# Kernel optimization log

Hardware: AMD Instinct MI355X
Metric: run time of the kernel (lower is better)

Reference implementation:

```python
import jax, jax.numpy as jnp
import numpy as np

ATOMS_PER_RES = 24  # hard-coded in .view(B, N_l, -1, 24)
NEG_SLOPE = 0.01    # nn.LeakyReLU default


def setup_inputs() -> dict:
    key = jax.random.key(0)
    ks = jax.random.split(key, 10)
    B, N_l, N_p, H, G = 16, 64, 512, 128, 10
    pos_l = jax.random.normal(ks[0], (B, N_l, 3), jnp.float32) * 5.0
    pos_p = jax.random.normal(ks[1], (B, N_p, ATOMS_PER_RES, 3), jnp.float32) * 5.0
    Interact = jax.random.normal(ks[2], (B, N_l, N_p, H), jnp.float32)
    Interact_mask = jax.random.randint(ks[3], (B, N_l, N_p), 0, 2) > 0
    W_pi = jax.random.normal(ks[4], (H, G), jnp.float32) * 0.05
    b_pi = jnp.zeros((G,), jnp.float32)
    W_sigma = jax.random.normal(ks[5], (H, G), jnp.float32) * 0.05
    b_sigma = jnp.zeros((G,), jnp.float32)
    W_mu = jax.random.normal(ks[6], (H, G), jnp.float32) * 0.05
    b_mu = jnp.zeros((G,), jnp.float32)
    return {
        "pos_l": pos_l, "pos_p": pos_p, "Interact": Interact,
        "Interact_mask": Interact_mask,
        "W_pi": W_pi, "b_pi": b_pi,
        "W_sigma": W_sigma, "b_sigma": b_sigma,
        "W_mu": W_mu, "b_mu": b_mu,
    }


def _min_dist(pos_l, pos_p):
    # pos_l: [B, N_l, 3]; pos_p: [B, N_p, 24, 3]
    B, N_l, _ = pos_l.shape
    Y = pos_p.reshape(B, -1, 3)  # [B, N_p*24, 3]
    d2 = (jnp.sum(pos_l * pos_l, axis=-1)[..., None]
          + jnp.sum(Y * Y, axis=-1)[:, None, :]
          - 2.0 * jnp.einsum('bic,bjc->bij', pos_l, Y))  # [B, N_l, N_p*24]
    dist = jnp.nan_to_num(jnp.sqrt(d2), nan=10000.0)
    # min over the 24 atoms of each residue -> [B, N_l, N_p]
    return dist.reshape(B, N_l, -1, ATOMS_PER_RES).min(axis=-1)


def reference(pos_l, pos_p, Interact, Interact_mask,
              W_pi, b_pi, W_sigma, b_sigma, W_mu, b_mu):
    leaky = lambda x: jax.nn.leaky_relu(x, NEG_SLOPE)
    dist = _min_dist(pos_l, pos_p)                       # [B, N_l, N_p]
    # original gathers dist[Interact_mask]; keep static shape, zero-fill masked-out
    dist_masked = jnp.where(Interact_mask, dist, 0.0)
    pi = jax.nn.softmax(Interact @ W_pi + b_pi, axis=-1)          # [B,N_l,N_p,G]
    sigma = jnp.clip(leaky(Interact @ W_sigma + b_sigma) + 1.1, 1e-6, None)
    mu = leaky(Interact @ W_mu + b_mu) + 1.0
    return pi, sigma, mu, dist_masked, Interact_mask
```

## Files before the change

### kernel.cpp

```cpp
#include <hip/hip_runtime.h>
#include <cmath>

#define NB 16
#define NL 64
#define NP 512
#define NH 128
#define NG 10
#define ROWS (NB * NL * NP)

#define OFF_PI    ((size_t)0)
#define OFF_SIGMA ((size_t)5242880)
#define OFF_MU    ((size_t)10485760)
#define OFF_DIST  ((size_t)15728640)
#define OFF_MASK  ((size_t)16252928)

typedef __attribute__((ext_vector_type(8))) short short8;
typedef __attribute__((ext_vector_type(4))) float f32x4;

__device__ __forceinline__ unsigned pk2(float a, float b) {
    unsigned ua = __float_as_uint(a);
    unsigned ub = __float_as_uint(b);
    ua = (ua + 0x7fffu + ((ua >> 16) & 1u)) >> 16;
    ub = (ub + 0x7fffu + ((ub >> 16) & 1u)) & 0xffff0000u;
    return ua | ub;
}

__global__ __launch_bounds__(512) void k_pack(
    const float* __restrict__ Wpi, const float* __restrict__ Wsg,
    const float* __restrict__ Wmu, uint4* __restrict__ tbl)
{
    int e    = threadIdx.x;
    int lane = e & 63;
    int n    = (e >> 6) & 1;
    int ks   = e >> 7;
    int lrow = lane & 15, lkg = lane >> 4;
    int col  = n * 16 + lrow;
    float w[8];
    #pragma unroll
    for (int j = 0; j < 8; ++j) {
        int k = ks * 32 + lkg * 8 + j;
        float v = 0.0f;
        if      (col < 10) v = Wpi[k * NG + col];
        else if (col < 20) v = Wsg[k * NG + col - 10];
        else if (col < 30) v = Wmu[k * NG + col - 20];
        w[j] = v;
    }
    uint4 u = {pk2(w[0], w[1]), pk2(w[2], w[3]),
               pk2(w[4], w[5]), pk2(w[6], w[7])};
    tbl[e] = u;
}

__global__ __launch_bounds__(256, 4) void k_fused(
    const float* __restrict__ pos_l,
    const float* __restrict__ pos_p,
    const int*   __restrict__ mask,
    const float* __restrict__ X,
    const uint4* __restrict__ wtbl,
    const float* __restrict__ bpi,
    const float* __restrict__ bsg,
    const float* __restrict__ bmu,
    float* __restrict__ out_pi,
    float* __restrict__ out_sg,
    float* __restrict__ out_mu,
    float* __restrict__ dist_out,
    float* __restrict__ mask_out)
{
    __shared__ __align__(16) float xs[256 * 32];
    __shared__ __align__(16) uint4 bt[512];

    const int tid  = threadIdx.x;
    const int wv   = tid >> 6;
    const int lane = tid & 63;
    const int lrow = lane & 15;
    const int lkg  = lane >> 4;
    const int idx  = blockIdx.x * 256 + tid;
    const size_t row0 = (size_t)blockIdx.x * 256;

    const int a_ = lane >> 3;
    const int b_ = lane & 7;
    const int wchunk = b_ ^ a_;
    const int wro    = wv * 8 + a_;
    const float* gsb = X + (row0 + wro) * NH + b_ * 4;

    uint4 bt0 = wtbl[tid];
    uint4 bt1 = wtbl[tid + 256];
    float4 pf[8];
    #pragma unroll
    for (int j = 0; j < 8; ++j)
        pf[j] = *(const float4*)(gsb + (size_t)j * 32 * NH);

    const int c0 = lrow, c1 = lrow + 16;
    const float bv0 = (c0 < 10) ? bpi[c0] : bsg[c0 - 10];
    const float bv1 = (c1 < 20) ? bsg[c1 - 10] : (c1 < 30 ? bmu[c1 - 20] : 0.0f);

    {
        int p  = idx & (NP - 1);
        int bl = idx >> 9;
        int b  = bl >> 6;

        const float* xl = pos_l + bl * 3;
        float x0 = xl[0], x1 = xl[1], x2 = xl[2];
        float qs = x0 * x0 + x1 * x1 + x2 * x2;

        const float4* yp = (const float4*)(pos_p + ((size_t)(b * NP + p)) * 72);

        float m2 = 1e30f;
        #pragma unroll
        for (int q = 0; q < 6; ++q) {
            float4 v0 = yp[q * 3 + 0];
            float4 v1 = yp[q * 3 + 1];
            float4 v2 = yp[q * 3 + 2];
            float c[12] = {v0.x, v0.y, v0.z, v0.w,
                           v1.x, v1.y, v1.z, v1.w,
                           v2.x, v2.y, v2.z, v2.w};
            #pragma unroll
            for (int a = 0; a < 4; ++a) {
                float yx = c[a * 3 + 0], yy = c[a * 3 + 1], yz = c[a * 3 + 2];
                float d2 = qs + (yx * yx + yy * yy + yz * yz)
                              - 2.0f * (x0 * yx + x1 * yy + x2 * yz);
                d2 = (d2 >= 0.0f) ? d2 : 1e8f;
                m2 = fminf(m2, d2);
            }
        }
        float m = sqrtf(m2);
        int mk = mask[idx];
        dist_out[idx] = mk ? m : 0.0f;
        mask_out[idx] = mk ? 1.0f : 0.0f;
    }

    bt[tid]       = bt0;
    bt[tid + 256] = bt1;
    #pragma unroll
    for (int j = 0; j < 8; ++j)
        *(float4*)&xs[(wro + j * 32) * 32 + wchunk * 4] = pf[j];
    __syncthreads();

    f32x4 acc[4][2];
    #pragma unroll
    for (int m = 0; m < 4; ++m) {
        acc[m][0] = (f32x4){bv0, bv0, bv0, bv0};
        acc[m][1] = (f32x4){bv1, bv1, bv1, bv1};
    }

    const int s7 = lrow & 7;
    #pragma unroll
    for (int t = 0; t < 4; ++t) {
        if (t < 3) {
            #pragma unroll
            for (int j = 0; j < 8; ++j)
                pf[j] = *(const float4*)(gsb + (size_t)j * 32 * NH
                                             + (t + 1) * 32);
        }
        short8 bf0 = __builtin_bit_cast(short8, bt[(t * 2 + 0) * 64 + lane]);
        short8 bf1 = __builtin_bit_cast(short8, bt[(t * 2 + 1) * 64 + lane]);

        #pragma unroll
        for (int m = 0; m < 4; ++m) {
            const int R = wv * 64 + m * 16 + lrow;
            float4 lo = *(const float4*)&xs[R * 32 + ((2 * lkg)     ^ s7) * 4];
            float4 hi = *(const float4*)&xs[R * 32 + ((2 * lkg + 1) ^ s7) * 4];
            uint4 ua = {pk2(lo.x, lo.y), pk2(lo.z, lo.w),
                        pk2(hi.x, hi.y), pk2(hi.z, hi.w)};
            short8 af = __builtin_bit_cast(short8, ua);
            acc[m][0] = __builtin_amdgcn_mfma_f32_16x16x32_bf16(af, bf0, acc[m][0], 0, 0, 0);
            acc[m][1] = __builtin_amdgcn_mfma_f32_16x16x32_bf16(af, bf1, acc[m][1], 0, 0, 0);
        }

        if (t < 3) {
            __syncthreads();
            #pragma unroll
            for (int j = 0; j < 8; ++j)
                *(float4*)&xs[(wro + j * 32) * 32 + wchunk * 4] = pf[j];
            __syncthreads();
        }
    }

    #pragma unroll
    for (int m = 0; m < 4; ++m)
        #pragma unroll
        for (int n = 0; n < 2; ++n)
            #pragma unroll
            for (int r = 0; r < 4; ++r) {
                int Rabs = wv * 64 + m * 16 + lkg * 4 + r;
                int ch   = n * 4 + (lrow >> 2);
                xs[Rabs * 32 + ((ch ^ (Rabs & 7)) * 4) + (lrow & 3)]
                    = acc[m][n][r];
            }

    float a[32];
    #pragma unroll
    for (int j = 0; j < 8; ++j)
        *(float4*)&a[4 * j] = *(const float4*)&xs[tid * 32 + ((j ^ (tid & 7)) * 4)];

    const size_t ro = (size_t)idx * NG;

    float mx = a[0];
    #pragma unroll
    for (int g = 1; g < NG; ++g) mx = fmaxf(mx, a[g]);
    float e[NG], ssum = 0.0f;
    #pragma unroll
    for (int g = 0; g < NG; ++g) { e[g] = __expf(a[g] - mx); ssum += e[g]; }
    float inv = 1.0f / ssum;
    #pragma unroll
    for (int g = 0; g < 5; ++g)
        *(float2*)&out_pi[ro + 2 * g] = make_float2(e[2 * g] * inv,
                                                    e[2 * g + 1] * inv);

    #pragma unroll
    for (int g = 0; g < 5; ++g) {
        float xa = a[10 + 2 * g], xb = a[10 + 2 * g + 1];
        float va = fmaxf((xa >= 0.0f ? xa : 0.01f * xa) + 1.1f, 1e-6f);
        float vb = fmaxf((xb >= 0.0f ? xb : 0.01f * xb) + 1.1f, 1e-6f);
        *(float2*)&out_sg[ro + 2 * g] = make_float2(va, vb);
    }

    #pragma unroll
    for (int g = 0; g < 5; ++g) {
        float xa = a[20 + 2 * g], xb = a[20 + 2 * g + 1];
        float va = (xa >= 0.0f ? xa : 0.01f * xa) + 1.0f;
        float vb = (xb >= 0.0f ? xb : 0.01f * xb) + 1.0f;
        *(float2*)&out_mu[ro + 2 * g] = make_float2(va, vb);
    }
}

extern "C" void kernel_launch(void* const* d_in, const int* in_sizes, int n_in,
                              void* d_out, int out_size, void* d_ws, size_t ws_size,
                              hipStream_t stream) {
    const float* pos_l    = (const float*)d_in[0];
    const float* pos_p    = (const float*)d_in[1];
    const float* Interact = (const float*)d_in[2];
    const int*   mask     = (const int*)  d_in[3];
    const float* Wpi      = (const float*)d_in[4];
    const float* bpi      = (const float*)d_in[5];
    const float* Wsg      = (const float*)d_in[6];
    const float* bsg      = (const float*)d_in[7];
    const float* Wmu      = (const float*)d_in[8];
    const float* bmu      = (const float*)d_in[9];

    float* out      = (float*)d_out;
    float* out_pi   = out + OFF_PI;
    float* out_sg   = out + OFF_SIGMA;
    float* out_mu   = out + OFF_MU;
    float* out_dist = out + OFF_DIST;
    float* out_mask = out + OFF_MASK;

    uint4* wtbl = (uint4*)d_ws;

    hipLaunchKernelGGL(k_pack, dim3(1), dim3(512), 0, stream,
                       Wpi, Wsg, Wmu, wtbl);
    hipLaunchKernelGGL(k_fused, dim3(ROWS / 256), dim3(256), 0, stream,
                       pos_l, pos_p, mask, Interact, wtbl,
                       bpi, bsg, bmu,
                       out_pi, out_sg, out_mu, out_dist, out_mask);
}
```

Baseline: 458.0 us.

## Stage bf16-packed activations in LDS in two halves, read weights from global

After: 432.0 us. 5.7% less time.

```diff
diff --git a/kernel.cpp b/kernel.cpp
--- a/kernel.cpp
+++ b/kernel.cpp
@@ -65,8 +65,8 @@
     float* __restrict__ dist_out,
     float* __restrict__ mask_out)
 {
-    __shared__ __align__(16) float xs[256 * 32];
-    __shared__ __align__(16) uint4 bt[512];
+    __shared__ __align__(16) char smem[32768];
+    float* cs = (float*)smem;
 
     const int tid  = threadIdx.x;
     const int wv   = tid >> 6;
@@ -76,22 +76,18 @@
     const int idx  = blockIdx.x * 256 + tid;
     const size_t row0 = (size_t)blockIdx.x * 256;
 
-    const int a_ = lane >> 3;
-    const int b_ = lane & 7;
-    const int wchunk = b_ ^ a_;
-    const int wro    = wv * 8 + a_;
-    const float* gsb = X + (row0 + wro) * NH + b_ * 4;
-
-    uint4 bt0 = wtbl[tid];
-    uint4 bt1 = wtbl[tid + 256];
-    float4 pf[8];
-    #pragma unroll
-    for (int j = 0; j < 8; ++j)
-        pf[j] = *(const float4*)(gsb + (size_t)j * 32 * NH);
-
-    const int c0 = lrow, c1 = lrow + 16;
-    const float bv0 = (c0 < 10) ? bpi[c0] : bsg[c0 - 10];
-    const float bv1 = (c1 < 20) ? bsg[c1 - 10] : (c1 < 30 ? bmu[c1 - 20] : 0.0f);
+    const int r0 = tid >> 4, c0 = tid & 15;
+    const float* gs = X + (row0 + r0) * NH + c0 * 4;
+    const int wbyte0 = r0 * 128 + ((((c0 >> 1) ^ (r0 & 7)) * 16) | ((c0 & 1) * 8));
+
+    float4 pf[16];
+    #pragma unroll
+    for (int j = 0; j < 16; ++j)
+        pf[j] = *(const float4*)(gs + (size_t)j * 16 * NH);
+
+    const int cc0 = lrow, cc1 = lrow + 16;
+    const float bv0 = (cc0 < 10) ? bpi[cc0] : bsg[cc0 - 10];
+    const float bv1 = (cc1 < 20) ? bsg[cc1 - 10] : (cc1 < 30 ? bmu[cc1 - 20] : 0.0f);
 
     {
         int p  = idx & (NP - 1);
@@ -128,11 +124,15 @@
         mask_out[idx] = mk ? 1.0f : 0.0f;
     }
 
-    bt[tid]       = bt0;
-    bt[tid + 256] = bt1;
-    #pragma unroll
-    for (int j = 0; j < 8; ++j)
-        *(float4*)&xs[(wro + j * 32) * 32 + wchunk * 4] = pf[j];
+    {
+        uint2 pc[16];
+        #pragma unroll
+        for (int j = 0; j < 16; ++j)
+            pc[j] = make_uint2(pk2(pf[j].x, pf[j].y), pk2(pf[j].z, pf[j].w));
+        #pragma unroll
+        for (int j = 0; j < 16; ++j)
+            *(uint2*)(smem + wbyte0 + j * 2048) = pc[j];
+    }
     __syncthreads();
 
     f32x4 acc[4][2];
@@ -143,37 +143,43 @@
     }
 
     const int s7 = lrow & 7;
-    #pragma unroll
-    for (int t = 0; t < 4; ++t) {
-        if (t < 3) {
-            #pragma unroll
-            for (int j = 0; j < 8; ++j)
-                pf[j] = *(const float4*)(gsb + (size_t)j * 32 * NH
-                                             + (t + 1) * 32);
-        }
-        short8 bf0 = __builtin_bit_cast(short8, bt[(t * 2 + 0) * 64 + lane]);
-        short8 bf1 = __builtin_bit_cast(short8, bt[(t * 2 + 1) * 64 + lane]);
-
-        #pragma unroll
-        for (int m = 0; m < 4; ++m) {
-            const int R = wv * 64 + m * 16 + lrow;
-            float4 lo = *(const float4*)&xs[R * 32 + ((2 * lkg)     ^ s7) * 4];
-            float4 hi = *(const float4*)&xs[R * 32 + ((2 * lkg + 1) ^ s7) * 4];
-            uint4 ua = {pk2(lo.x, lo.y), pk2(lo.z, lo.w),
-                        pk2(hi.x, hi.y), pk2(hi.z, hi.w)};
-            short8 af = __builtin_bit_cast(short8, ua);
-            acc[m][0] = __builtin_amdgcn_mfma_f32_16x16x32_bf16(af, bf0, acc[m][0], 0, 0, 0);
-            acc[m][1] = __builtin_amdgcn_mfma_f32_16x16x32_bf16(af, bf1, acc[m][1], 0, 0, 0);
-        }
-
-        if (t < 3) {
-            __syncthreads();
-            #pragma unroll
-            for (int j = 0; j < 8; ++j)
-                *(float4*)&xs[(wro + j * 32) * 32 + wchunk * 4] = pf[j];
-            __syncthreads();
-        }
-    }
+    const char* abase = smem + wv * 8192 + lrow * 128;
+
+#define DO_KS(ksg, Cb)                                                        \
+    {                                                                         \
+        short8 bf0 = __builtin_bit_cast(short8, wtbl[((ksg) * 2 + 0) * 64 + lane]); \
+        short8 bf1 = __builtin_bit_cast(short8, wtbl[((ksg) * 2 + 1) * 64 + lane]); \
+        _Pragma("unroll")                                                     \
+        for (int m = 0; m < 4; ++m) {                                         \
+            short8 af = *(const short8*)(abase + m * 2048                     \
+                                         + ((((Cb)) ^ s7) * 16));             \
+            acc[m][0] = __builtin_amdgcn_mfma_f32_16x16x32_bf16(af, bf0, acc[m][0], 0, 0, 0); \
+            acc[m][1] = __builtin_amdgcn_mfma_f32_16x16x32_bf16(af, bf1, acc[m][1], 0, 0, 0); \
+        }                                                                     \
+    }
+
+    DO_KS(0, lkg)
+
+    #pragma unroll
+    for (int j = 0; j < 16; ++j)
+        pf[j] = *(const float4*)(gs + (size_t)j * 16 * NH + 64);
+
+    DO_KS(1, 4 + lkg)
+
+    uint2 pc[16];
+    #pragma unroll
+    for (int j = 0; j < 16; ++j)
+        pc[j] = make_uint2(pk2(pf[j].x, pf[j].y), pk2(pf[j].z, pf[j].w));
+
+    __syncthreads();
+    #pragma unroll
+    for (int j = 0; j < 16; ++j)
+        *(uint2*)(smem + wbyte0 + j * 2048) = pc[j];
+    __syncthreads();
+
+    DO_KS(2, lkg)
+    DO_KS(3, 4 + lkg)
+#undef DO_KS
 
     #pragma unroll
     for (int m = 0; m < 4; ++m)
@@ -183,14 +189,14 @@
             for (int r = 0; r < 4; ++r) {
                 int Rabs = wv * 64 + m * 16 + lkg * 4 + r;
                 int ch   = n * 4 + (lrow >> 2);
-                xs[Rabs * 32 + ((ch ^ (Rabs & 7)) * 4) + (lrow & 3)]
+                cs[Rabs * 32 + ((ch ^ (Rabs & 7)) * 4) + (lrow & 3)]
                     = acc[m][n][r];
             }
 
     float a[32];
     #pragma unroll
     for (int j = 0; j < 8; ++j)
-        *(float4*)&a[4 * j] = *(const float4*)&xs[tid * 32 + ((j ^ (tid & 7)) * 4)];
+        *(float4*)&a[4 * j] = *(const float4*)&cs[tid * 32 + ((j ^ (tid & 7)) * 4)];
 
     const size_t ro = (size_t)idx * NG;
 
```
